# Kernel tuning notes

Measured on AMD Instinct MI355X. Metric: run time of the kernel, lower is better.

The kernel has to match this reference:

```python
import jax, jax.numpy as jnp
import numpy as np

NEG_SLOPE = 0.01  # nn.LeakyReLU default

N = 100000
E = 1600000
D_IN = 128
D_OUT = 128


def setup_inputs() -> dict:
    key = jax.random.key(0)
    ks = jax.random.split(key, 8)
    features = jax.random.normal(ks[0], (N, D_IN), dtype=jnp.float32)
    adj_rows = jax.random.randint(ks[1], (E,), 0, N, dtype=jnp.int64)
    adj_cols = jax.random.randint(ks[2], (E,), 0, N, dtype=jnp.int64)
    adj_vals = jax.random.uniform(ks[3], (E,), dtype=jnp.float32)
    s1 = 1.0 / np.sqrt(D_IN)
    W1 = jax.random.uniform(ks[4], (D_IN, D_OUT), jnp.float32, -s1, s1)
    b1 = jax.random.uniform(ks[5], (D_OUT,), jnp.float32, -s1, s1)
    W2 = jax.random.uniform(ks[6], (D_IN, D_OUT), jnp.float32, -s1, s1)
    b2 = jax.random.uniform(ks[7], (D_OUT,), jnp.float32, -s1, s1)
    return {"features": features, "adj_rows": adj_rows, "adj_cols": adj_cols,
            "adj_vals": adj_vals, "W1": W1, "b1": b1, "W2": W2, "b2": b2}


def reference(features, adj_rows, adj_cols, adj_vals, W1, b1, W2, b2):
    # h_neigh = adj @ features  (COO SpMM via gather + segment_sum)
    msgs = adj_vals[:, None] * features[adj_cols]          # [E, D_IN]
    h_neigh = jax.ops.segment_sum(msgs, adj_rows, num_segments=features.shape[0])
    term1 = (features + h_neigh) @ W1 + b1                 # W1(features + h_neigh)
    term2 = (features * h_neigh) @ W2 + b2                 # W2(features * h_neigh)
    pre = term1 + term2
    return jnp.where(pre >= 0, pre, NEG_SLOPE * pre)       # leaky_relu
```

## Files before the change

### kernel.cpp

```cpp
#include <hip/hip_runtime.h>

#define D 128
#define BM 64

typedef short short8 __attribute__((ext_vector_type(8)));
typedef unsigned short ushort8_t __attribute__((ext_vector_type(8)));
typedef float f32x4 __attribute__((ext_vector_type(4)));

__device__ __forceinline__ unsigned short f2bf(float x) {
    unsigned u = __float_as_uint(x);
    unsigned r = (u + 0x7fffu + ((u >> 16) & 1u)) >> 16;
    return (unsigned short)r;
}
__device__ __forceinline__ float bf2f(unsigned short u) {
    return __uint_as_float(((unsigned)u) << 16);
}

__global__ __launch_bounds__(256) void prep_kernel(
    const float4* __restrict__ feat4, ushort4* __restrict__ fbf4, int nf4,
    const float* __restrict__ W1, const float* __restrict__ W2,
    unsigned short* __restrict__ WT,
    const int* __restrict__ rows, int* __restrict__ bcnt,
    int E, int nb, int epb)
{
    __shared__ int cnt[1024];
    const int t = threadIdx.x;
    const int b = blockIdx.x;
    for (int i = t; i < nb; i += 256) cnt[i] = 0;
    __syncthreads();

    int e0 = b * epb;
    int e1 = e0 + epb; if (e1 > E) e1 = E;
    for (int e = e0 + t; e < e1; e += 256) atomicAdd(&cnt[rows[e] >> 7], 1);

    for (int i = b * 256 + t; i < nf4; i += 256 * 256) {
        float4 v = feat4[i];
        fbf4[i] = make_ushort4(f2bf(v.x), f2bf(v.y), f2bf(v.z), f2bf(v.w));
    }

    if (b < 128) {
        int idx = b * 256 + t;
        int c = idx & 127;
        int k = idx >> 7;
        float w = (k < 128) ? W1[k * 128 + c] : W2[(k - 128) * 128 + c];
        WT[c * 256 + k] = f2bf(w);
    }

    __syncthreads();
    for (int i = t; i < nb; i += 256)
        if (cnt[i]) atomicAdd(&bcnt[i], cnt[i]);
}

__global__ __launch_bounds__(256) void fconv_kernel(
    const float4* __restrict__ feat4, ushort4* __restrict__ fbf4, int total)
{
    int i = blockIdx.x * 256 + threadIdx.x;
    if (i < total) {
        float4 v = feat4[i];
        fbf4[i] = make_ushort4(f2bf(v.x), f2bf(v.y), f2bf(v.z), f2bf(v.w));
    }
}

__global__ __launch_bounds__(256) void wconv_kernel(
    const float* __restrict__ W1, const float* __restrict__ W2,
    unsigned short* __restrict__ WT)
{
    int idx = blockIdx.x * 256 + threadIdx.x;
    int c = idx & 127;
    int k = idx >> 7;
    float w = (k < 128) ? W1[k * 128 + c] : W2[(k - 128) * 128 + c];
    WT[c * 256 + k] = f2bf(w);
}

__global__ __launch_bounds__(1024) void bucket_scan_kernel(
    const int* __restrict__ bcnt, int* __restrict__ bstart,
    int* __restrict__ bcur, int nb, int E)
{
    __shared__ int wsum[16];
    int tid = threadIdx.x, lane = tid & 63, wid = tid >> 6;
    int x = (tid < nb) ? bcnt[tid] : 0;
    int v = x;
    #pragma unroll
    for (int off = 1; off < 64; off <<= 1) {
        int y = __shfl_up(v, off, 64);
        if (lane >= off) v += y;
    }
    if (lane == 63) wsum[wid] = v;
    __syncthreads();
    if (wid == 0 && lane < 16) {
        int s = wsum[lane];
        #pragma unroll
        for (int off = 1; off < 16; off <<= 1) {
            int y = __shfl_up(s, off, 64);
            if (lane >= off) s += y;
        }
        wsum[lane] = s;
    }
    __syncthreads();
    int wexcl = wid ? wsum[wid - 1] : 0;
    int excl = wexcl + v - x;
    if (tid < nb) { bstart[tid] = excl; bcur[tid] = excl; }
    if (tid == 0) bstart[nb] = E;
}

__global__ __launch_bounds__(256) void bucket_scatter_kernel(
    const int* __restrict__ rows, const int* __restrict__ cols,
    const float* __restrict__ vals, int* __restrict__ bcur,
    uint2* __restrict__ bsedge, int E, int nb)
{
    __shared__ int cnt[1024];
    __shared__ int base[1024];
    int t = threadIdx.x;
    int e0 = blockIdx.x * 4096;
    for (int i = t; i < nb; i += 256) cnt[i] = 0;
    __syncthreads();
    #pragma unroll
    for (int q = 0; q < 16; ++q) {
        int e = e0 + t + q * 256;
        if (e < E) atomicAdd(&cnt[rows[e] >> 7], 1);
    }
    __syncthreads();
    for (int i = t; i < nb; i += 256) {
        int c = cnt[i];
        if (c) { base[i] = atomicAdd(&bcur[i], c); cnt[i] = 0; }
    }
    __syncthreads();
    #pragma unroll
    for (int q = 0; q < 16; ++q) {
        int e = e0 + t + q * 256;
        if (e < E) {
            int r = rows[e];
            int b = r >> 7;
            int pos = base[b] + atomicAdd(&cnt[b], 1);
            bsedge[pos] = make_uint2(((unsigned)(r & 127) << 17) | (unsigned)cols[e],
                                     __float_as_uint(vals[e]));
        }
    }
}

__global__ __launch_bounds__(256) void bucket_sort_kernel(
    const uint2* __restrict__ bsedge,
    const int* __restrict__ bstart,
    uint2* __restrict__ sedge,
    int* __restrict__ row_start,
    int N, int E)
{
    __shared__ int cnt[128];
    __shared__ int base[128];
    const int b = blockIdx.x;
    const int t = threadIdx.x;
    const int s = bstart[b], e = bstart[b + 1];
    if (t < 128) cnt[t] = 0;
    __syncthreads();
    for (int j = s + t; j < e; j += 256)
        atomicAdd(&cnt[bsedge[j].x >> 17], 1);
    __syncthreads();
    if (t < 64) {
        int c0 = cnt[2 * t], c1 = cnt[2 * t + 1];
        int pair = c0 + c1;
        int v = pair;
        #pragma unroll
        for (int off = 1; off < 64; off <<= 1) {
            int y = __shfl_up(v, off, 64);
            if (t >= off) v += y;
        }
        int excl = v - pair;
        base[2 * t]     = excl;
        base[2 * t + 1] = excl + c0;
        cnt[2 * t] = 0;
        cnt[2 * t + 1] = 0;
    }
    __syncthreads();
    const int r0 = b << 7;
    if (t < 128 && r0 + t < N) row_start[r0 + t] = s + base[t];
    if (b == 0 && t == 0) row_start[N] = E;
    for (int j = s + t; j < e; j += 256) {
        uint2 ed = bsedge[j];
        int rl = ed.x >> 17;
        int p = atomicAdd(&cnt[rl], 1);
        sedge[s + base[rl] + p] = make_uint2(ed.x & 0x1FFFFu, ed.y);
    }
}

__global__ __launch_bounds__(256) void spmm_ab_kernel(
    const ushort8_t* __restrict__ fbf8,
    const int* __restrict__ row_start,
    const uint2* __restrict__ sedge,
    unsigned char* __restrict__ ambf, int N)
{
    int t = blockIdx.x * 256 + threadIdx.x;
    int row = t >> 4;
    int l   = t & 15;
    if (row >= N) return;

    int s = row_start[row];
    int e = row_start[row + 1];

    float acc[8] = {};
    int j = s;
    for (; j + 3 < e; j += 4) {
        uint2 e0 = sedge[j],     e1 = sedge[j + 1];
        uint2 e2 = sedge[j + 2], e3 = sedge[j + 3];
        ushort8_t f0 = fbf8[(size_t)e0.x * 16 + l];
        ushort8_t f1 = fbf8[(size_t)e1.x * 16 + l];
        ushort8_t f2 = fbf8[(size_t)e2.x * 16 + l];
        ushort8_t f3 = fbf8[(size_t)e3.x * 16 + l];
        float v0 = __uint_as_float(e0.y), v1 = __uint_as_float(e1.y);
        float v2 = __uint_as_float(e2.y), v3 = __uint_as_float(e3.y);
        #pragma unroll
        for (int q = 0; q < 8; ++q) {
            acc[q] = fmaf(v0, bf2f(f0[q]), acc[q]);
            acc[q] = fmaf(v1, bf2f(f1[q]), acc[q]);
            acc[q] = fmaf(v2, bf2f(f2[q]), acc[q]);
            acc[q] = fmaf(v3, bf2f(f3[q]), acc[q]);
        }
    }
    for (; j < e; ++j) {
        uint2 e0 = sedge[j];
        float v = __uint_as_float(e0.y);
        ushort8_t f0 = fbf8[(size_t)e0.x * 16 + l];
        #pragma unroll
        for (int q = 0; q < 8; ++q) acc[q] = fmaf(v, bf2f(f0[q]), acc[q]);
    }

    ushort8_t fown = fbf8[(size_t)row * 16 + l];
    ushort8_t av, mv;
    #pragma unroll
    for (int q = 0; q < 8; ++q) {
        float f = bf2f(fown[q]);
        av[q] = f2bf(f + acc[q]);
        mv[q] = f2bf(f * acc[q]);
    }

    int swz = (row & 7) << 4;
    unsigned char* rowp = ambf + (size_t)row * 512;
    *(ushort8_t*)(rowp + ((16 * l) ^ swz))       = av;
    *(ushort8_t*)(rowp + 256 + ((16 * l) ^ swz)) = mv;
}

__global__ __launch_bounds__(256) void mfma_gemm2_kernel(
    const unsigned char* __restrict__ ambf,
    const unsigned short* __restrict__ WT,
    const float* __restrict__ b1, const float* __restrict__ b2,
    float* __restrict__ out, int N)
{
    __shared__ __align__(16) unsigned char am_raw[64 * 512];

    const int tid = threadIdx.x;
    const int block0 = blockIdx.x * BM;

    const short8* src = (const short8*)(ambf + (size_t)block0 * 512);
    short8* dst = (short8*)am_raw;
    #pragma unroll
    for (int it = 0; it < 8; ++it) {
        int idx = tid + it * 256;
        dst[idx] = src[idx];
    }
    __syncthreads();

    const int lane = tid & 63;
    const int w    = tid >> 6;
    const int wr   = w >> 1;
    const int wc   = w & 1;
    const int l15  = lane & 15;
    const int lk   = lane >> 4;
    const int rswz = (l15 & 7) << 4;

    f32x4 acc[2][4] = {};

    const char* WTc = (const char*)WT;
    const unsigned char* arow0 = am_raw + (wr * 32 + l15) * 512;
    const unsigned char* arow1 = arow0 + 16 * 512;

    #pragma unroll
    for (int ks = 0; ks < 8; ++ks) {
        int kbyte = ks * 64 + lk * 16;
        int akoff = kbyte ^ rswz;
        short8 a0 = *(const short8*)(arow0 + akoff);
        short8 a1 = *(const short8*)(arow1 + akoff);
        short8 bfr[4];
        #pragma unroll
        for (int nc = 0; nc < 4; ++nc) {
            int col = wc * 64 + nc * 16 + l15;
            bfr[nc] = *(const short8*)(WTc + col * 512 + kbyte);
        }
        #pragma unroll
        for (int nc = 0; nc < 4; ++nc) {
            acc[0][nc] = __builtin_amdgcn_mfma_f32_16x16x32_bf16(a0, bfr[nc], acc[0][nc], 0, 0, 0);
            acc[1][nc] = __builtin_amdgcn_mfma_f32_16x16x32_bf16(a1, bfr[nc], acc[1][nc], 0, 0, 0);
        }
    }

    #pragma unroll
    for (int nc = 0; nc < 4; ++nc) {
        int col = wc * 64 + nc * 16 + l15;
        float bias = b1[col] + b2[col];
        #pragma unroll
        for (int mr = 0; mr < 2; ++mr) {
            int rbase = block0 + wr * 32 + mr * 16 + lk * 4;
            #pragma unroll
            for (int r = 0; r < 4; ++r) {
                int row = rbase + r;
                if (row < N) {
                    float v = acc[mr][nc][r] + bias;
                    out[row * 128 + col] = (v >= 0.f) ? v : 0.01f * v;
                }
            }
        }
    }
}

__global__ __launch_bounds__(256) void hist_kernel(
    const int* __restrict__ rows, int* __restrict__ counts, int E)
{
    int e = blockIdx.x * 256 + threadIdx.x;
    if (e < E) atomicAdd(&counts[rows[e]], 1);
}

__global__ __launch_bounds__(256) void scan_pass1(
    const int* __restrict__ counts, int* __restrict__ btot, int N)
{
    int tid = threadIdx.x;
    int i = blockIdx.x * 1024 + tid * 4;
    int s = 0;
    if (i + 3 < N) {
        int4 v = *(const int4*)(counts + i);
        s = v.x + v.y + v.z + v.w;
    } else {
        for (int q = 0; q < 4; ++q) if (i + q < N) s += counts[i + q];
    }
    #pragma unroll
    for (int off = 32; off >= 1; off >>= 1) s += __shfl_down(s, off, 64);
    __shared__ int ws[4];
    if ((tid & 63) == 0) ws[tid >> 6] = s;
    __syncthreads();
    if (tid == 0) btot[blockIdx.x] = ws[0] + ws[1] + ws[2] + ws[3];
}

__global__ __launch_bounds__(1024) void scan_pass2(
    const int* __restrict__ btot, int* __restrict__ boff, int nb)
{
    __shared__ int wsum[16];
    int tid = threadIdx.x, lane = tid & 63, wid = tid >> 6;
    int x = (tid < nb) ? btot[tid] : 0;
    int v = x;
    #pragma unroll
    for (int off = 1; off < 64; off <<= 1) {
        int y = __shfl_up(v, off, 64);
        if (lane >= off) v += y;
    }
    if (lane == 63) wsum[wid] = v;
    __syncthreads();
    if (wid == 0 && lane < 16) {
        int s = wsum[lane];
        #pragma unroll
        for (int off = 1; off < 16; off <<= 1) {
            int y = __shfl_up(s, off, 64);
            if (lane >= off) s += y;
        }
        wsum[lane] = s;
    }
    __syncthreads();
    int wexcl = wid ? wsum[wid - 1] : 0;
    if (tid < nb) boff[tid] = wexcl + v - x;
}

__global__ __launch_bounds__(256) void scan_pass3(
    int* __restrict__ row_start, int* __restrict__ cursor,
    const int* __restrict__ boff, int N, int E)
{
    int tid = threadIdx.x;
    int base = blockIdx.x * 1024 + tid * 4;
    int c0 = 0, c1 = 0, c2 = 0, c3 = 0;
    if (base + 3 < N) {
        int4 v = *(const int4*)(row_start + base);
        c0 = v.x; c1 = v.y; c2 = v.z; c3 = v.w;
    } else {
        if (base + 0 < N) c0 = row_start[base + 0];
        if (base + 1 < N) c1 = row_start[base + 1];
        if (base + 2 < N) c2 = row_start[base + 2];
        if (base + 3 < N) c3 = row_start[base + 3];
    }
    int s0 = c0, s1 = s0 + c1, s2 = s1 + c2, s3 = s2 + c3;
    int lane = tid & 63, wid = tid >> 6;
    int v = s3;
    #pragma unroll
    for (int off = 1; off < 64; off <<= 1) {
        int y = __shfl_up(v, off, 64);
        if (lane >= off) v += y;
    }
    __shared__ int ws[4];
    if (lane == 63) ws[wid] = v;
    __syncthreads();
    int wexcl = 0;
    for (int q = 0; q < wid; ++q) wexcl += ws[q];
    int texcl = wexcl + (v - s3) + boff[blockIdx.x];
    int e0 = texcl, e1 = texcl + s0, e2 = texcl + s1, e3 = texcl + s2;
    if (base + 0 < N) { row_start[base + 0] = e0; cursor[base + 0] = e0; }
    if (base + 1 < N) { row_start[base + 1] = e1; cursor[base + 1] = e1; }
    if (base + 2 < N) { row_start[base + 2] = e2; cursor[base + 2] = e2; }
    if (base + 3 < N) { row_start[base + 3] = e3; cursor[base + 3] = e3; }
    if (blockIdx.x == 0 && tid == 0) row_start[N] = E;
}

__global__ __launch_bounds__(256) void scatter_sort_kernel(
    const int* __restrict__ rows, const int* __restrict__ cols,
    const float* __restrict__ vals, int* __restrict__ cursor,
    uint2* __restrict__ sedge, int E)
{
    int e = blockIdx.x * 256 + threadIdx.x;
    if (e < E) {
        int r = rows[e];
        int p = atomicAdd(&cursor[r], 1);
        sedge[p] = make_uint2((unsigned)cols[e], __float_as_uint(vals[e]));
    }
}

__global__ __launch_bounds__(256) void spmm_kernel(
    const float2* __restrict__ feat2,
    const int* __restrict__ row_start,
    const uint2* __restrict__ sedge,
    float2* __restrict__ h2, int N)
{
    int gw = (blockIdx.x * 256 + threadIdx.x) >> 6;
    int lane = threadIdx.x & 63;
    if (gw >= N) return;
    int s = row_start[gw];
    int e = row_start[gw + 1];
    float2 acc = make_float2(0.f, 0.f);
    int j = s;
    for (; j + 1 < e; j += 2) {
        uint2 e0 = sedge[j], e1 = sedge[j + 1];
        float v0 = __uint_as_float(e0.y), v1 = __uint_as_float(e1.y);
        float2 f0 = feat2[(size_t)e0.x * 64 + lane];
        float2 f1 = feat2[(size_t)e1.x * 64 + lane];
        acc.x = fmaf(v0, f0.x, acc.x);
        acc.y = fmaf(v0, f0.y, acc.y);
        acc.x = fmaf(v1, f1.x, acc.x);
        acc.y = fmaf(v1, f1.y, acc.y);
    }
    if (j < e) {
        uint2 e0 = sedge[j];
        float v = __uint_as_float(e0.y);
        float2 f = feat2[(size_t)e0.x * 64 + lane];
        acc.x = fmaf(v, f.x, acc.x);
        acc.y = fmaf(v, f.y, acc.y);
    }
    h2[(size_t)gw * 64 + lane] = acc;
}

__global__ __launch_bounds__(256) void mfma_gemm_kernel(
    const float4* __restrict__ feat4, const float4* __restrict__ h4,
    const unsigned short* __restrict__ WT,
    const float* __restrict__ b1, const float* __restrict__ b2,
    float* __restrict__ out, int N)
{
    __shared__ __align__(16) unsigned char am_raw[64 * 512];
    const int tid = threadIdx.x;
    const int block0 = blockIdx.x * BM;
    #pragma unroll
    for (int it = 0; it < 8; ++it) {
        int idx  = tid + it * 256;
        int node = idx >> 5;
        int p    = idx & 31;
        int g    = block0 + node;
        float4 fv = make_float4(0.f, 0.f, 0.f, 0.f);
        float4 hv = make_float4(0.f, 0.f, 0.f, 0.f);
        if (g < N) { fv = feat4[g * 32 + p]; hv = h4[g * 32 + p]; }
        ushort4 av = make_ushort4(f2bf(fv.x + hv.x), f2bf(fv.y + hv.y),
                                  f2bf(fv.z + hv.z), f2bf(fv.w + hv.w));
        ushort4 mv = make_ushort4(f2bf(fv.x * hv.x), f2bf(fv.y * hv.y),
                                  f2bf(fv.z * hv.z), f2bf(fv.w * hv.w));
        int swz = (node & 7) << 4;
        *(ushort4*)(am_raw + node * 512 + ((p * 8) ^ swz))       = av;
        *(ushort4*)(am_raw + node * 512 + ((256 + p * 8) ^ swz)) = mv;
    }
    __syncthreads();
    const int lane = tid & 63;
    const int w    = tid >> 6;
    const int wr   = w >> 1;
    const int wc   = w & 1;
    const int l15  = lane & 15;
    const int lk   = lane >> 4;
    const int rswz = (l15 & 7) << 4;
    f32x4 acc[2][4] = {};
    const char* WTc = (const char*)WT;
    const unsigned char* arow0 = am_raw + (wr * 32 + l15) * 512;
    const unsigned char* arow1 = arow0 + 16 * 512;
    #pragma unroll
    for (int ks = 0; ks < 8; ++ks) {
        int kbyte = ks * 64 + lk * 16;
        int akoff = kbyte ^ rswz;
        short8 a0 = *(const short8*)(arow0 + akoff);
        short8 a1 = *(const short8*)(arow1 + akoff);
        short8 bfr[4];
        #pragma unroll
        for (int nc = 0; nc < 4; ++nc) {
            int col = wc * 64 + nc * 16 + l15;
            bfr[nc] = *(const short8*)(WTc + col * 512 + kbyte);
        }
        #pragma unroll
        for (int nc = 0; nc < 4; ++nc) {
            acc[0][nc] = __builtin_amdgcn_mfma_f32_16x16x32_bf16(a0, bfr[nc], acc[0][nc], 0, 0, 0);
            acc[1][nc] = __builtin_amdgcn_mfma_f32_16x16x32_bf16(a1, bfr[nc], acc[1][nc], 0, 0, 0);
        }
    }
    #pragma unroll
    for (int nc = 0; nc < 4; ++nc) {
        int col = wc * 64 + nc * 16 + l15;
        float bias = b1[col] + b2[col];
        #pragma unroll
        for (int mr = 0; mr < 2; ++mr) {
            int rbase = block0 + wr * 32 + mr * 16 + lk * 4;
            #pragma unroll
            for (int r = 0; r < 4; ++r) {
                int row = rbase + r;
                if (row < N) {
                    float v = acc[mr][nc][r] + bias;
                    out[row * 128 + col] = (v >= 0.f) ? v : 0.01f * v;
                }
            }
        }
    }
}

__global__ __launch_bounds__(256) void edge_scatter_kernel(
    const float4* __restrict__ feat4, const int* __restrict__ rows,
    const int* __restrict__ cols, const float* __restrict__ vals,
    float* __restrict__ h, int E)
{
    int idx = blockIdx.x * 256 + threadIdx.x;
    if (idx >= E * 32) return;
    int e = idx >> 5;
    int p = idx & 31;
    int r = rows[e];
    int c = cols[e];
    float v = vals[e];
    float4 f = feat4[c * 32 + p];
    float* hr = h + (long long)r * D + p * 4;
    unsafeAtomicAdd(hr + 0, v * f.x);
    unsafeAtomicAdd(hr + 1, v * f.y);
    unsafeAtomicAdd(hr + 2, v * f.z);
    unsafeAtomicAdd(hr + 3, v * f.w);
}

__global__ __launch_bounds__(256) void fused_gemm_kernel(
    const float* __restrict__ feat, const float* __restrict__ h,
    const float* __restrict__ W1, const float* __restrict__ b1,
    const float* __restrict__ W2, const float* __restrict__ b2,
    float* __restrict__ out, int N)
{
    __shared__ float a_lds[BM][D];
    __shared__ float m_lds[BM][D];
    const int tid = threadIdx.x;
    const int block0 = blockIdx.x * BM;
    const float4* feat4 = (const float4*)feat;
    const float4* h4    = (const float4*)h;
    #pragma unroll
    for (int it = 0; it < 8; ++it) {
        int idx  = tid + it * 256;
        int node = idx >> 5;
        int p    = idx & 31;
        int gnode = block0 + node;
        float4 fv = make_float4(0.f, 0.f, 0.f, 0.f);
        float4 hv = make_float4(0.f, 0.f, 0.f, 0.f);
        if (gnode < N) { fv = feat4[gnode * 32 + p]; hv = h4[gnode * 32 + p]; }
        float4 av = make_float4(fv.x + hv.x, fv.y + hv.y, fv.z + hv.z, fv.w + hv.w);
        float4 mv = make_float4(fv.x * hv.x, fv.y * hv.y, fv.z * hv.z, fv.w * hv.w);
        *(float4*)&a_lds[node][p * 4] = av;
        *(float4*)&m_lds[node][p * 4] = mv;
    }
    __syncthreads();
    const int c = tid & 31;
    const int g = tid >> 5;
    float acc[8][4] = {};
    const float4* W1v = (const float4*)W1;
    const float4* W2v = (const float4*)W2;
    for (int k = 0; k < D; ++k) {
        float4 w1 = W1v[k * 32 + c];
        float4 w2 = W2v[k * 32 + c];
        #pragma unroll
        for (int t = 0; t < 8; ++t) {
            float av = a_lds[g + 8 * t][k];
            float mv = m_lds[g + 8 * t][k];
            acc[t][0] = fmaf(av, w1.x, fmaf(mv, w2.x, acc[t][0]));
            acc[t][1] = fmaf(av, w1.y, fmaf(mv, w2.y, acc[t][1]));
            acc[t][2] = fmaf(av, w1.z, fmaf(mv, w2.z, acc[t][2]));
            acc[t][3] = fmaf(av, w1.w, fmaf(mv, w2.w, acc[t][3]));
        }
    }
    float4 bb1 = ((const float4*)b1)[c];
    float4 bb2 = ((const float4*)b2)[c];
    const float bx = bb1.x + bb2.x, by = bb1.y + bb2.y;
    const float bz = bb1.z + bb2.z, bw = bb1.w + bb2.w;
    #pragma unroll
    for (int t = 0; t < 8; ++t) {
        int gnode = block0 + g + 8 * t;
        if (gnode >= N) continue;
        float4 o;
        o.x = acc[t][0] + bx; o.y = acc[t][1] + by;
        o.z = acc[t][2] + bz; o.w = acc[t][3] + bw;
        o.x = (o.x >= 0.f) ? o.x : 0.01f * o.x;
        o.y = (o.y >= 0.f) ? o.y : 0.01f * o.y;
        o.z = (o.z >= 0.f) ? o.z : 0.01f * o.z;
        o.w = (o.w >= 0.f) ? o.w : 0.01f * o.w;
        ((float4*)out)[gnode * 32 + c] = o;
    }
}

extern "C" void kernel_launch(void* const* d_in, const int* in_sizes, int n_in,
                              void* d_out, int out_size, void* d_ws, size_t ws_size,
                              hipStream_t stream) {
    const float* feat = (const float*)d_in[0];
    const int*   rows = (const int*)d_in[1];
    const int*   cols = (const int*)d_in[2];
    const float* vals = (const float*)d_in[3];
    const float* W1   = (const float*)d_in[4];
    const float* b1   = (const float*)d_in[5];
    const float* W2   = (const float*)d_in[6];
    const float* b2   = (const float*)d_in[7];

    const int N = in_sizes[0] / D;
    const int E = in_sizes[1];
    float* out = (float*)d_out;

    const int NBK  = (N + 127) >> 7;
    const int Npad = NBK << 7;

    size_t off = 0;
    unsigned char* ambf = (unsigned char*)d_ws;                    off += (size_t)Npad * 512;
    unsigned short* featbf = (unsigned short*)((char*)d_ws + off); off += (size_t)N * D * 2;
    off = (off + 15) & ~(size_t)15;
    uint2* sedge = (uint2*)((char*)d_ws + off);                    off += (size_t)E * 8;
    unsigned short* WT = (unsigned short*)((char*)d_ws + off);     off += 128 * 256 * 2;
    int* row_start = (int*)((char*)d_ws + off);                    off += (size_t)(N + 1) * 4;
    off = (off + 15) & ~(size_t)15;
    uint2* bsedge = (uint2*)((char*)d_ws + off);                   off += (size_t)E * 8;
    int* bcnt   = (int*)((char*)d_ws + off);                       off += (size_t)NBK * 4;
    int* bstart = (int*)((char*)d_ws + off);                       off += (size_t)(NBK + 1) * 4;
    int* bcur   = (int*)((char*)d_ws + off);                       off += (size_t)NBK * 4;
    size_t need1a = off;

    if (ws_size >= need1a && NBK <= 1024 && N <= (1 << 17)) {
        hipMemsetAsync(bcnt, 0, (size_t)NBK * sizeof(int), stream);
        int epb = (E + 255) / 256;
        prep_kernel<<<256, 256, 0, stream>>>(
            (const float4*)feat, (ushort4*)featbf, N * 32,
            W1, W2, WT, rows, bcnt, E, NBK, epb);
        bucket_scan_kernel<<<1, 1024, 0, stream>>>(bcnt, bstart, bcur, NBK, E);
        bucket_scatter_kernel<<<(E + 4095) / 4096, 256, 0, stream>>>(
            rows, cols, vals, bcur, bsedge, E, NBK);
        bucket_sort_kernel<<<NBK, 256, 0, stream>>>(
            bsedge, bstart, sedge, row_start, N, E);
        spmm_ab_kernel<<<(N * 16 + 255) / 256, 256, 0, stream>>>(
            (const ushort8_t*)featbf, row_start, sedge, ambf, N);
        mfma_gemm2_kernel<<<(N + BM - 1) / BM, 256, 0, stream>>>(
            ambf, WT, b1, b2, out, N);
        return;
    }

    const int NB = (N + 1023) / 1024;
    off = 0;
    ambf = (unsigned char*)d_ws;                                   off += (size_t)Npad * 512;
    featbf = (unsigned short*)((char*)d_ws + off);                 off += (size_t)N * D * 2;
    off = (off + 15) & ~(size_t)15;
    sedge = (uint2*)((char*)d_ws + off);                           off += (size_t)E * 8;
    WT = (unsigned short*)((char*)d_ws + off);                     off += 128 * 256 * 2;
    row_start = (int*)((char*)d_ws + off);                         off += (size_t)(N + 1) * 4;
    off = (off + 15) & ~(size_t)15;
    int* cursor = (int*)((char*)d_ws + off);                       off += (size_t)N * 4;
    int* btot = (int*)((char*)d_ws + off);                         off += (size_t)NB * 4;
    int* boff = (int*)((char*)d_ws + off);                         off += (size_t)NB * 4;
    size_t need1b = off;

    if (ws_size >= need1b && NB <= 1024) {
        hipMemsetAsync(row_start, 0, (size_t)(N + 1) * sizeof(int), stream);
        fconv_kernel<<<(N * 32 + 255) / 256, 256, 0, stream>>>(
            (const float4*)feat, (ushort4*)featbf, N * 32);
        wconv_kernel<<<128, 256, 0, stream>>>(W1, W2, WT);
        hist_kernel<<<(E + 255) / 256, 256, 0, stream>>>(rows, row_start, E);
        scan_pass1<<<NB, 256, 0, stream>>>(row_start, btot, N);
        scan_pass2<<<1, 1024, 0, stream>>>(btot, boff, NB);
        scan_pass3<<<NB, 256, 0, stream>>>(row_start, cursor, boff, N, E);
        scatter_sort_kernel<<<(E + 255) / 256, 256, 0, stream>>>(
            rows, cols, vals, cursor, sedge, E);
        spmm_ab_kernel<<<(N * 16 + 255) / 256, 256, 0, stream>>>(
            (const ushort8_t*)featbf, row_start, sedge, ambf, N);
        mfma_gemm2_kernel<<<(N + BM - 1) / BM, 256, 0, stream>>>(
            ambf, WT, b1, b2, out, N);
        return;
    }

    off = 0;
    float* h = (float*)d_ws;                           off += (size_t)N * D * 4;
    int* row_start2 = (int*)((char*)d_ws + off);       off += (size_t)(N + 1) * 4;
    int* cursor2    = (int*)((char*)d_ws + off);       off += (size_t)N * 4;
    off = (off + 15) & ~(size_t)15;
    uint2* sedge2   = (uint2*)((char*)d_ws + off);     off += (size_t)E * 8;
    off = (off + 15) & ~(size_t)15;
    unsigned short* WT2 = (unsigned short*)((char*)d_ws + off); off += 128 * 256 * 2;
    int* btot2 = (int*)((char*)d_ws + off);            off += (size_t)NB * 4;
    int* boff2 = (int*)((char*)d_ws + off);            off += (size_t)NB * 4;
    size_t need2 = off;

    if (ws_size >= need2 && NB <= 1024) {
        hipMemsetAsync(row_start2, 0, (size_t)(N + 1) * sizeof(int), stream);
        wconv_kernel<<<128, 256, 0, stream>>>(W1, W2, WT2);
        hist_kernel<<<(E + 255) / 256, 256, 0, stream>>>(rows, row_start2, E);
        scan_pass1<<<NB, 256, 0, stream>>>(row_start2, btot2, N);
        scan_pass2<<<1, 1024, 0, stream>>>(btot2, boff2, NB);
        scan_pass3<<<NB, 256, 0, stream>>>(row_start2, cursor2, boff2, N, E);
        scatter_sort_kernel<<<(E + 255) / 256, 256, 0, stream>>>(
            rows, cols, vals, cursor2, sedge2, E);
        spmm_kernel<<<(N * 64 + 255) / 256, 256, 0, stream>>>(
            (const float2*)feat, row_start2, sedge2, (float2*)h, N);
        mfma_gemm_kernel<<<(N + BM - 1) / BM, 256, 0, stream>>>(
            (const float4*)feat, (const float4*)h, WT2, b1, b2, out, N);
        return;
    }

    size_t hbytes = (size_t)N * D * sizeof(float);
    float* hh = (ws_size >= hbytes) ? (float*)d_ws : out;
    hipMemsetAsync(hh, 0, hbytes, stream);
    edge_scatter_kernel<<<((size_t)E * 32 + 255) / 256, 256, 0, stream>>>(
        (const float4*)feat, rows, cols, vals, hh, E);
    fused_gemm_kernel<<<(N + BM - 1) / BM, 256, 0, stream>>>(
        feat, hh, W1, b1, W2, b2, out, N);
}
```

Measured before the change: 193.0 us.

## Fuse per-bucket row sort into SpMM using 64-row buckets sorted in LDS

Bucket size drops from 128 to 64 rows, so there are twice as many buckets, and the scan now handles two buckets per thread. The separate bucket_sort and spmm kernels are merged into one kernel. It counting-sorts each bucket's edges into shared memory and then runs the gather-accumulate for its 64 rows straight from LDS. This removes the global round trip for sorted edges and row_start along with one kernel launch. In exchange, buckets that overflow the 1792-edge LDS capacity fall back to a slow scan of the whole bucket per row, and occupancy is limited by the 14KB LDS per 512-thread block.

After: 189.3 us. About the same (-1.9%).

```diff
diff --git a/kernel.cpp b/kernel.cpp
--- a/kernel.cpp
+++ b/kernel.cpp
@@ -2,6 +2,7 @@
 
 #define D 128
 #define BM 64
+#define CAP2 1792
 
 typedef short short8 __attribute__((ext_vector_type(8)));
 typedef unsigned short ushort8_t __attribute__((ext_vector_type(8)));
@@ -23,7 +24,7 @@
     const int* __restrict__ rows, int* __restrict__ bcnt,
     int E, int nb, int epb)
 {
-    __shared__ int cnt[1024];
+    __shared__ int cnt[2048];
     const int t = threadIdx.x;
     const int b = blockIdx.x;
     for (int i = t; i < nb; i += 256) cnt[i] = 0;
@@ -31,7 +32,7 @@
 
     int e0 = b * epb;
     int e1 = e0 + epb; if (e1 > E) e1 = E;
-    for (int e = e0 + t; e < e1; e += 256) atomicAdd(&cnt[rows[e] >> 7], 1);
+    for (int e = e0 + t; e < e1; e += 256) atomicAdd(&cnt[rows[e] >> 6], 1);
 
     for (int i = b * 256 + t; i < nf4; i += 256 * 256) {
         float4 v = feat4[i];
@@ -72,14 +73,17 @@
     WT[c * 256 + k] = f2bf(w);
 }
 
-__global__ __launch_bounds__(1024) void bucket_scan_kernel(
+__global__ __launch_bounds__(1024) void bucket_scan2_kernel(
     const int* __restrict__ bcnt, int* __restrict__ bstart,
     int* __restrict__ bcur, int nb, int E)
 {
     __shared__ int wsum[16];
     int tid = threadIdx.x, lane = tid & 63, wid = tid >> 6;
-    int x = (tid < nb) ? bcnt[tid] : 0;
-    int v = x;
+    int i0 = 2 * tid, i1 = 2 * tid + 1;
+    int x0 = (i0 < nb) ? bcnt[i0] : 0;
+    int x1 = (i1 < nb) ? bcnt[i1] : 0;
+    int s = x0 + x1;
+    int v = s;
     #pragma unroll
     for (int off = 1; off < 64; off <<= 1) {
         int y = __shfl_up(v, off, 64);
@@ -88,18 +92,19 @@
     if (lane == 63) wsum[wid] = v;
     __syncthreads();
     if (wid == 0 && lane < 16) {
-        int s = wsum[lane];
+        int w = wsum[lane];
         #pragma unroll
         for (int off = 1; off < 16; off <<= 1) {
-            int y = __shfl_up(s, off, 64);
-            if (lane >= off) s += y;
-        }
-        wsum[lane] = s;
+            int y = __shfl_up(w, off, 64);
+            if (lane >= off) w += y;
+        }
+        wsum[lane] = w;
     }
     __syncthreads();
     int wexcl = wid ? wsum[wid - 1] : 0;
-    int excl = wexcl + v - x;
-    if (tid < nb) { bstart[tid] = excl; bcur[tid] = excl; }
+    int excl = wexcl + v - s;
+    if (i0 < nb) { bstart[i0] = excl;      bcur[i0] = excl; }
+    if (i1 < nb) { bstart[i1] = excl + x0; bcur[i1] = excl + x0; }
     if (tid == 0) bstart[nb] = E;
 }
 
@@ -108,8 +113,8 @@
     const float* __restrict__ vals, int* __restrict__ bcur,
     uint2* __restrict__ bsedge, int E, int nb)
 {
-    __shared__ int cnt[1024];
-    __shared__ int base[1024];
+    __shared__ int cnt[2048];
+    __shared__ int base[2048];
     int t = threadIdx.x;
     int e0 = blockIdx.x * 4096;
     for (int i = t; i < nb; i += 256) cnt[i] = 0;
@@ -117,7 +122,7 @@
     #pragma unroll
     for (int q = 0; q < 16; ++q) {
         int e = e0 + t + q * 256;
-        if (e < E) atomicAdd(&cnt[rows[e] >> 7], 1);
+        if (e < E) atomicAdd(&cnt[rows[e] >> 6], 1);
     }
     __syncthreads();
     for (int i = t; i < nb; i += 256) {
@@ -130,112 +135,137 @@
         int e = e0 + t + q * 256;
         if (e < E) {
             int r = rows[e];
-            int b = r >> 7;
+            int b = r >> 6;
             int pos = base[b] + atomicAdd(&cnt[b], 1);
-            bsedge[pos] = make_uint2(((unsigned)(r & 127) << 17) | (unsigned)cols[e],
+            bsedge[pos] = make_uint2(((unsigned)(r & 63) << 17) | (unsigned)cols[e],
                                      __float_as_uint(vals[e]));
         }
     }
 }
 
-__global__ __launch_bounds__(256) void bucket_sort_kernel(
+__global__ __launch_bounds__(512) void spmm_sort64_kernel(
+    const ushort8_t* __restrict__ fbf8,
+    const int* __restrict__ bstart,
     const uint2* __restrict__ bsedge,
-    const int* __restrict__ bstart,
-    uint2* __restrict__ sedge,
-    int* __restrict__ row_start,
-    int N, int E)
-{
-    __shared__ int cnt[128];
-    __shared__ int base[128];
+    unsigned char* __restrict__ ambf, int N)
+{
+    __shared__ uint2 sL[CAP2];
+    __shared__ int cnt[64];
+    __shared__ int base[65];
+
+    const int t = threadIdx.x;
     const int b = blockIdx.x;
-    const int t = threadIdx.x;
     const int s = bstart[b], e = bstart[b + 1];
-    if (t < 128) cnt[t] = 0;
-    __syncthreads();
-    for (int j = s + t; j < e; j += 256)
+    const int M = e - s;
+
+    if (t < 64) cnt[t] = 0;
+    __syncthreads();
+    for (int j = s + t; j < e; j += 512)
         atomicAdd(&cnt[bsedge[j].x >> 17], 1);
     __syncthreads();
     if (t < 64) {
-        int c0 = cnt[2 * t], c1 = cnt[2 * t + 1];
-        int pair = c0 + c1;
-        int v = pair;
+        int c = cnt[t];
+        int v = c;
         #pragma unroll
         for (int off = 1; off < 64; off <<= 1) {
             int y = __shfl_up(v, off, 64);
             if (t >= off) v += y;
         }
-        int excl = v - pair;
-        base[2 * t]     = excl;
-        base[2 * t + 1] = excl + c0;
-        cnt[2 * t] = 0;
-        cnt[2 * t + 1] = 0;
-    }
-    __syncthreads();
-    const int r0 = b << 7;
-    if (t < 128 && r0 + t < N) row_start[r0 + t] = s + base[t];
-    if (b == 0 && t == 0) row_start[N] = E;
-    for (int j = s + t; j < e; j += 256) {
-        uint2 ed = bsedge[j];
-        int rl = ed.x >> 17;
-        int p = atomicAdd(&cnt[rl], 1);
-        sedge[s + base[rl] + p] = make_uint2(ed.x & 0x1FFFFu, ed.y);
-    }
-}
-
-__global__ __launch_bounds__(256) void spmm_ab_kernel(
-    const ushort8_t* __restrict__ fbf8,
-    const int* __restrict__ row_start,
-    const uint2* __restrict__ sedge,
-    unsigned char* __restrict__ ambf, int N)
-{
-    int t = blockIdx.x * 256 + threadIdx.x;
-    int row = t >> 4;
-    int l   = t & 15;
-    if (row >= N) return;
-
-    int s = row_start[row];
-    int e = row_start[row + 1];
-
-    float acc[8] = {};
-    int j = s;
-    for (; j + 3 < e; j += 4) {
-        uint2 e0 = sedge[j],     e1 = sedge[j + 1];
-        uint2 e2 = sedge[j + 2], e3 = sedge[j + 3];
-        ushort8_t f0 = fbf8[(size_t)e0.x * 16 + l];
-        ushort8_t f1 = fbf8[(size_t)e1.x * 16 + l];
-        ushort8_t f2 = fbf8[(size_t)e2.x * 16 + l];
-        ushort8_t f3 = fbf8[(size_t)e3.x * 16 + l];
-        float v0 = __uint_as_float(e0.y), v1 = __uint_as_float(e1.y);
-        float v2 = __uint_as_float(e2.y), v3 = __uint_as_float(e3.y);
-        #pragma unroll
-        for (int q = 0; q < 8; ++q) {
-            acc[q] = fmaf(v0, bf2f(f0[q]), acc[q]);
-            acc[q] = fmaf(v1, bf2f(f1[q]), acc[q]);
-            acc[q] = fmaf(v2, bf2f(f2[q]), acc[q]);
-            acc[q] = fmaf(v3, bf2f(f3[q]), acc[q]);
-        }
-    }
-    for (; j < e; ++j) {
-        uint2 e0 = sedge[j];
-        float v = __uint_as_float(e0.y);
-        ushort8_t f0 = fbf8[(size_t)e0.x * 16 + l];
-        #pragma unroll
-        for (int q = 0; q < 8; ++q) acc[q] = fmaf(v, bf2f(f0[q]), acc[q]);
-    }
-
-    ushort8_t fown = fbf8[(size_t)row * 16 + l];
-    ushort8_t av, mv;
-    #pragma unroll
-    for (int q = 0; q < 8; ++q) {
-        float f = bf2f(fown[q]);
-        av[q] = f2bf(f + acc[q]);
-        mv[q] = f2bf(f * acc[q]);
-    }
-
-    int swz = (row & 7) << 4;
-    unsigned char* rowp = ambf + (size_t)row * 512;
-    *(ushort8_t*)(rowp + ((16 * l) ^ swz))       = av;
-    *(ushort8_t*)(rowp + 256 + ((16 * l) ^ swz)) = mv;
+        base[t] = v - c;
+        if (t == 63) base[64] = v;
+        cnt[t] = 0;
+    }
+    __syncthreads();
+
+    const int g = t >> 4;
+    const int l = t & 15;
+    const int row0 = b << 6;
+
+    if (M <= CAP2) {
+        for (int j = s + t; j < e; j += 512) {
+            uint2 ed = bsedge[j];
+            int rl = ed.x >> 17;
+            int p = atomicAdd(&cnt[rl], 1);
+            sL[base[rl] + p] = make_uint2(ed.x & 0x1FFFFu, ed.y);
+        }
+        __syncthreads();
+
+        #pragma unroll
+        for (int rr = 0; rr < 2; ++rr) {
+            int r6 = g + rr * 32;
+            int row = row0 + r6;
+            if (row >= N) continue;
+            int j  = base[r6];
+            int j1 = base[r6 + 1];
+            float acc[8] = {};
+            for (; j + 3 < j1; j += 4) {
+                uint2 e0 = sL[j],     e1 = sL[j + 1];
+                uint2 e2 = sL[j + 2], e3 = sL[j + 3];
+                ushort8_t f0 = fbf8[(size_t)e0.x * 16 + l];
+                ushort8_t f1 = fbf8[(size_t)e1.x * 16 + l];
+                ushort8_t f2 = fbf8[(size_t)e2.x * 16 + l];
+                ushort8_t f3 = fbf8[(size_t)e3.x * 16 + l];
+                float v0 = __uint_as_float(e0.y), v1 = __uint_as_float(e1.y);
+                float v2 = __uint_as_float(e2.y), v3 = __uint_as_float(e3.y);
+                #pragma unroll
+                for (int q = 0; q < 8; ++q) {
+                    acc[q] = fmaf(v0, bf2f(f0[q]), acc[q]);
+                    acc[q] = fmaf(v1, bf2f(f1[q]), acc[q]);
+                    acc[q] = fmaf(v2, bf2f(f2[q]), acc[q]);
+                    acc[q] = fmaf(v3, bf2f(f3[q]), acc[q]);
+                }
+            }
+            for (; j < j1; ++j) {
+                uint2 e0 = sL[j];
+                float v = __uint_as_float(e0.y);
+                ushort8_t f0 = fbf8[(size_t)e0.x * 16 + l];
+                #pragma unroll
+                for (int q = 0; q < 8; ++q) acc[q] = fmaf(v, bf2f(f0[q]), acc[q]);
+            }
+
+            ushort8_t fown = fbf8[(size_t)row * 16 + l];
+            ushort8_t av, mv;
+            #pragma unroll
+            for (int q = 0; q < 8; ++q) {
+                float f = bf2f(fown[q]);
+                av[q] = f2bf(f + acc[q]);
+                mv[q] = f2bf(f * acc[q]);
+            }
+            int swz = (row & 7) << 4;
+            unsigned char* rowp = ambf + (size_t)row * 512;
+            *(ushort8_t*)(rowp + ((16 * l) ^ swz))       = av;
+            *(ushort8_t*)(rowp + 256 + ((16 * l) ^ swz)) = mv;
+        }
+    } else {
+        #pragma unroll
+        for (int rr = 0; rr < 2; ++rr) {
+            int r6 = g + rr * 32;
+            int row = row0 + r6;
+            if (row >= N) continue;
+            float acc[8] = {};
+            for (int j = s; j < e; ++j) {
+                uint2 ed = bsedge[j];
+                if ((int)(ed.x >> 17) == r6) {
+                    float v = __uint_as_float(ed.y);
+                    ushort8_t f0 = fbf8[(size_t)(ed.x & 0x1FFFFu) * 16 + l];
+                    #pragma unroll
+                    for (int q = 0; q < 8; ++q) acc[q] = fmaf(v, bf2f(f0[q]), acc[q]);
+                }
+            }
+            ushort8_t fown = fbf8[(size_t)row * 16 + l];
+            ushort8_t av, mv;
+            #pragma unroll
+            for (int q = 0; q < 8; ++q) {
+                float f = bf2f(fown[q]);
+                av[q] = f2bf(f + acc[q]);
+                mv[q] = f2bf(f * acc[q]);
+            }
+            int swz = (row & 7) << 4;
+            unsigned char* rowp = ambf + (size_t)row * 512;
+            *(ushort8_t*)(rowp + ((16 * l) ^ swz))       = av;
+            *(ushort8_t*)(rowp + 256 + ((16 * l) ^ swz)) = mv;
+        }
+    }
 }
 
 __global__ __launch_bounds__(256) void mfma_gemm2_kernel(
@@ -624,73 +654,38 @@
     const int E = in_sizes[1];
     float* out = (float*)d_out;
 
-    const int NBK  = (N + 127) >> 7;
-    const int Npad = NBK << 7;
+    const int NBK  = (N + 63) >> 6;
+    const int Npad = NBK << 6;
 
     size_t off = 0;
     unsigned char* ambf = (unsigned char*)d_ws;                    off += (size_t)Npad * 512;
     unsigned short* featbf = (unsigned short*)((char*)d_ws + off); off += (size_t)N * D * 2;
     off = (off + 15) & ~(size_t)15;
-    uint2* sedge = (uint2*)((char*)d_ws + off);                    off += (size_t)E * 8;
     unsigned short* WT = (unsigned short*)((char*)d_ws + off);     off += 128 * 256 * 2;
-    int* row_start = (int*)((char*)d_ws + off);                    off += (size_t)(N + 1) * 4;
     off = (off + 15) & ~(size_t)15;
     uint2* bsedge = (uint2*)((char*)d_ws + off);                   off += (size_t)E * 8;
     int* bcnt   = (int*)((char*)d_ws + off);                       off += (size_t)NBK * 4;
     int* bstart = (int*)((char*)d_ws + off);                       off += (size_t)(NBK + 1) * 4;
     int* bcur   = (int*)((char*)d_ws + off);                       off += (size_t)NBK * 4;
-    size_t need1a = off;
-
-    if (ws_size >= need1a && NBK <= 1024 && N <= (1 << 17)) {
+    size_t need1 = off;
+
+    if (ws_size >= need1 && NBK <= 2048 && N <= (1 << 17)) {
         hipMemsetAsync(bcnt, 0, (size_t)NBK * sizeof(int), stream);
         int epb = (E + 255) / 256;
         prep_kernel<<<256, 256, 0, stream>>>(
             (const float4*)feat, (ushort4*)featbf, N * 32,
             W1, W2, WT, rows, bcnt, E, NBK, epb);
-        bucket_scan_kernel<<<1, 1024, 0, stream>>>(bcnt, bstart, bcur, NBK, E);
+        bucket_scan2_kernel<<<1, 1024, 0, stream>>>(bcnt, bstart, bcur, NBK, E);
         bucket_scatter_kernel<<<(E + 4095) / 4096, 256, 0, stream>>>(
             rows, cols, vals, bcur, bsedge, E, NBK);
-        bucket_sort_kernel<<<NBK, 256, 0, stream>>>(
-            bsedge, bstart, sedge, row_start, N, E);
-        spmm_ab_kernel<<<(N * 16 + 255) / 256, 256, 0, stream>>>(
-            (const ushort8_t*)featbf, row_start, sedge, ambf, N);
+        spmm_sort64_kernel<<<NBK, 512, 0, stream>>>(
+            (const ushort8_t*)featbf, bstart, bsedge, ambf, N);
         mfma_gemm2_kernel<<<(N + BM - 1) / BM, 256, 0, stream>>>(
             ambf, WT, b1, b2, out, N);
         return;
     }
 
     const int NB = (N + 1023) / 1024;
-    off = 0;
-    ambf = (unsigned char*)d_ws;                                   off += (size_t)Npad * 512;
-    featbf = (unsigned short*)((char*)d_ws + off);                 off += (size_t)N * D * 2;
-    off = (off + 15) & ~(size_t)15;
-    sedge = (uint2*)((char*)d_ws + off);                           off += (size_t)E * 8;
-    WT = (unsigned short*)((char*)d_ws + off);                     off += 128 * 256 * 2;
-    row_start = (int*)((char*)d_ws + off);                         off += (size_t)(N + 1) * 4;
-    off = (off + 15) & ~(size_t)15;
-    int* cursor = (int*)((char*)d_ws + off);                       off += (size_t)N * 4;
-    int* btot = (int*)((char*)d_ws + off);                         off += (size_t)NB * 4;
-    int* boff = (int*)((char*)d_ws + off);                         off += (size_t)NB * 4;
-    size_t need1b = off;
-
-    if (ws_size >= need1b && NB <= 1024) {
-        hipMemsetAsync(row_start, 0, (size_t)(N + 1) * sizeof(int), stream);
-        fconv_kernel<<<(N * 32 + 255) / 256, 256, 0, stream>>>(
-            (const float4*)feat, (ushort4*)featbf, N * 32);
-        wconv_kernel<<<128, 256, 0, stream>>>(W1, W2, WT);
-        hist_kernel<<<(E + 255) / 256, 256, 0, stream>>>(rows, row_start, E);
-        scan_pass1<<<NB, 256, 0, stream>>>(row_start, btot, N);
-        scan_pass2<<<1, 1024, 0, stream>>>(btot, boff, NB);
-        scan_pass3<<<NB, 256, 0, stream>>>(row_start, cursor, boff, N, E);
-        scatter_sort_kernel<<<(E + 255) / 256, 256, 0, stream>>>(
-            rows, cols, vals, cursor, sedge, E);
-        spmm_ab_kernel<<<(N * 16 + 255) / 256, 256, 0, stream>>>(
-            (const ushort8_t*)featbf, row_start, sedge, ambf, N);
-        mfma_gemm2_kernel<<<(N + BM - 1) / BM, 256, 0, stream>>>(
-            ambf, WT, b1, b2, out, N);
-        return;
-    }
-
     off = 0;
     float* h = (float*)d_ws;                           off += (size_t)N * D * 4;
     int* row_start2 = (int*)((char*)d_ws + off);       off += (size_t)(N + 1) * 4;
```
